# Kernel optimization log

Measured on AMD Instinct MI355X. Metric: run time of the kernel, lower is better.

Reference implementation:

```python
import jax, jax.numpy as jnp
import numpy as np

VOCAB = 150
EOS = 2
PAD = 0
EPS = 1e-8


def _ngram_penalty_sum(tokens, n):
    # tokens: [B, S] int. Returns sum over batch of (count-2)*0.1*n for each
    # ngram repeated >=3 times. Equivalent trick: hash each ngram to a unique
    # int (base-VOCAB encoding), sort per row; a position is a 3rd-or-later
    # occurrence iff sorted[i] == sorted[i-2]; the number of such positions
    # equals sum over unique ngrams of max(count-2, 0).
    B, S = tokens.shape
    if S < n * 3:
        return jnp.float32(0.0)
    L = S - n + 1
    h = sum(tokens[:, j:j + L].astype(jnp.int32) * (VOCAB ** j) for j in range(n))
    hs = jnp.sort(h, axis=1)
    rep = jnp.sum(hs[:, 2:] == hs[:, :-2], axis=1)  # [B]
    return jnp.sum(rep.astype(jnp.float32)) * (0.1 * n)


def setup_inputs() -> dict:
    key = jax.random.key(0)
    k1, k2, k3 = jax.random.split(key, 3)
    B, S, V, IN = 256, 512, VOCAB, 512
    predictions = jax.random.normal(k1, (B, S, V), dtype=jnp.float32)
    targets = jax.random.randint(k2, (B, S), 0, V)
    attention_weights = jax.random.uniform(k3, (B, S, IN), dtype=jnp.float32)
    return {"predictions": predictions, "targets": targets,
            "attention_weights": attention_weights}


def reference(predictions, targets, attention_weights):
    B, S, V = predictions.shape

    # --- main NLL loss (ignore_index=PAD, mean over non-pad) ---
    mask = (targets != PAD).astype(predictions.dtype)  # [B,S]
    gathered = jnp.take_along_axis(predictions, targets[..., None], axis=-1)[..., 0]
    main = -jnp.sum(gathered * mask) / jnp.maximum(jnp.sum(mask), 1.0)

    # --- pattern penalty on argmax tokens ---
    pred_tokens = jnp.argmax(predictions, axis=-1)  # [B,S]
    pattern = (_ngram_penalty_sum(pred_tokens, 2)
               + _ngram_penalty_sum(pred_tokens, 3)
               + _ngram_penalty_sum(pred_tokens, 4)) / B

    # --- EOS encouragement ---
    eos_mask = (targets == EOS).astype(predictions.dtype)  # [B,S]
    eos_probs = jax.nn.softmax(predictions, axis=-1)[:, :, EOS]  # [B,S]
    eos_loss = -jnp.mean(eos_mask * jnp.log(eos_probs + EPS))
    eos_loss = jnp.where(jnp.sum(eos_mask) > 0, eos_loss, 0.0)
    has_eos_t = jnp.any(targets == EOS, axis=1)
    has_eos_p = jnp.any(pred_tokens == EOS, axis=1)
    no_eos = jnp.mean((has_eos_t & ~has_eos_p).astype(predictions.dtype))
    eos_total = eos_loss + 0.5 * no_eos

    # --- attention diversity (negative mean entropy, scaled) ---
    ent = -jnp.sum(attention_weights * jnp.log(attention_weights + EPS), axis=-1)
    attention = -jnp.mean(ent) * 0.1

    total = main + 0.1 * pattern + 0.2 * eos_total + 0.05 * attention
    return jnp.stack([total, main, pattern, eos_total, attention])
```

## Files before the change

### kernel.cpp

```cpp
#include <hip/hip_runtime.h>
#include <math.h>

#define BB   256
#define SS   512
#define VV   150
#define NPOS (BB * SS)
#define GRID 2048
#define EPSF 1e-8f


__device__ __forceinline__ unsigned key32(float f, int idx) {
    const unsigned u = __float_as_uint(f);
    const unsigned mono = ((int)u >= 0) ? (u | 0x80000000u) : ~u;
    return (mono & 0xFFFFFF00u) | (unsigned)(255 - idx);
}

__global__ __launch_bounds__(256) void kern_ab(
    const float* __restrict__ pred, const int* __restrict__ tgt,
    const float* __restrict__ attw, float4* __restrict__ pA,
    float* __restrict__ pB, unsigned char* __restrict__ toks,
    int* __restrict__ counter)
{
    __shared__ float shp[16];
    __shared__ float shb[4];
    const int tid  = threadIdx.x;
    const int lane = tid & 63;
    const int wid  = tid >> 6;

    if (blockIdx.x == 0 && tid == 0) *counter = 0;

    const int gw = blockIdx.x * 4 + wid;
    const float4* a4 = (const float4*)attw;
    const size_t bbase = (size_t)blockIdx.x * 8192;

    float s_g = 0.f, s_mc = 0.f, s_el = 0.f, s_ec = 0.f;
    float s0 = 0.f, s1 = 0.f;

    for (int it = 0; it < 16; ++it) {
        const float4 x0 = a4[bbase + (size_t)(2 * it)     * 256 + tid];
        const float4 x1 = a4[bbase + (size_t)(2 * it + 1) * 256 + tid];

        const int pos = gw + it * 8192;
        const float* row = pred + (size_t)pos * VV;
        const float v0 = row[lane];
        const float v1 = row[lane + 64];
        const bool  l3 = lane < (VV - 128);
        const float v2 = l3 ? row[lane + 128] : -INFINITY;

        unsigned k = key32(v0, lane);
        k = max(k, key32(v1, lane + 64));
        if (l3) k = max(k, key32(v2, lane + 128));
        #pragma unroll
        for (int off = 32; off > 0; off >>= 1)
            k = max(k, __shfl_xor(k, off));
        const int li = 255 - (int)(k & 0xFFu);

        const int t = tgt[pos];
        const float src = (t < 64) ? v0 : (t < 128) ? v1 : v2;
        const float g = __shfl(src, t & 63);

        if (t == 2) {
            const unsigned mono_hi = k & 0xFFFFFF00u;
            const float m = (mono_hi & 0x80000000u)
                          ? __uint_as_float(mono_hi & 0x7FFFFFFFu)
                          : __uint_as_float(~mono_hi);
            float ex = __expf(v0 - m) + __expf(v1 - m)
                     + (l3 ? __expf(v2 - m) : 0.f);
            #pragma unroll
            for (int off = 32; off > 0; off >>= 1)
                ex += __shfl_xor(ex, off);
            const float p2 = __shfl(v0, 2);
            if (lane == 0) {
                s_el += __logf(__expf(p2 - m) / ex + EPSF);
                s_ec += 1.f;
            }
        }
        if (lane == 0) {
            toks[pos] = (unsigned char)li;
            if (t != 0) { s_g += g; s_mc += 1.f; }
        }

        s0 += x0.x * __logf(x0.x + EPSF) + x0.y * __logf(x0.y + EPSF)
            + x0.z * __logf(x0.z + EPSF) + x0.w * __logf(x0.w + EPSF);
        s1 += x1.x * __logf(x1.x + EPSF) + x1.y * __logf(x1.y + EPSF)
            + x1.z * __logf(x1.z + EPSF) + x1.w * __logf(x1.w + EPSF);
    }

    if (lane == 0) {
        shp[wid * 4 + 0] = s_g;  shp[wid * 4 + 1] = s_mc;
        shp[wid * 4 + 2] = s_el; shp[wid * 4 + 3] = s_ec;
    }
    float s = s0 + s1;
    #pragma unroll
    for (int off = 32; off > 0; off >>= 1) s += __shfl_xor(s, off);
    if (lane == 0) shb[wid] = s;

    __syncthreads();
    if (tid == 0) {
        float4 r;
        r.x = shp[0] + shp[4] + shp[8]  + shp[12];
        r.y = shp[1] + shp[5] + shp[9]  + shp[13];
        r.z = shp[2] + shp[6] + shp[10] + shp[14];
        r.w = shp[3] + shp[7] + shp[11] + shp[15];
        pA[blockIdx.x] = r;
        pB[blockIdx.x] = shb[0] + shb[1] + shb[2] + shb[3];
    }
}

__global__ __launch_bounds__(256) void kern_cf(
    const unsigned char* __restrict__ toks, const int* __restrict__ tgt,
    int* __restrict__ pC, int* __restrict__ hasx, int* __restrict__ counter,
    const float4* __restrict__ pA, const float* __restrict__ pB,
    float* __restrict__ out)
{
    const int blk = blockIdx.x;
    const int b = blk & 255;
    const int n = 2 + (blk >> 8);
    const int L = SS - n + 1;
    const int tid = threadIdx.x;

    __shared__ int tok[SS];
    __shared__ __align__(16) int h[SS];
    __shared__ int sflags;
    __shared__ int sticket;

    if (tid == 0) sflags = 0;
    const unsigned char* rt = toks + b * SS;
    tok[tid]       = rt[tid];
    tok[tid + 256] = rt[tid + 256];
    __syncthreads();

    if (blk < 256) {
        const int* trow = tgt + b * SS;
        int f = 0;
        if (trow[tid] == 2 || trow[tid + 256] == 2) f |= 1;
        if (tok[tid] == 2 || tok[tid + 256] == 2)   f |= 2;
        if (f) atomicOr(&sflags, f);
    }

    #pragma unroll
    for (int q = 0; q < 2; ++q) {
        const int i = tid + q * 256;
        int hv;
        if (i < L) {
            hv = tok[i];
            int mul = VV;
            for (int j = 1; j < n; ++j) { hv += tok[i + j] * mul; mul *= VV; }
        } else {
            hv = 0x7F000000 + i;
        }
        h[i] = hv;
    }
    __syncthreads();

    const int i1 = tid, i2 = tid + 256;
    const int h1 = h[i1], h2 = h[i2];
    const int bound1 = (i1 & ~3) + 4;
    const int bound2 = (i2 & ~3) + 4;
    int c1 = 0, c2 = 0;
    for (int j = 0; j < bound1; j += 4) {
        const int4 hv = *(const int4*)&h[j];
        c1 += (hv.x == h1 && j     < i1) + (hv.y == h1 && j + 1 < i1)
            + (hv.z == h1 && j + 2 < i1) + (hv.w == h1 && j + 3 < i1);
    }
    for (int j = 0; j < bound2; j += 4) {
        const int4 hv = *(const int4*)&h[j];
        c2 += (hv.x == h2 && j     < i2) + (hv.y == h2 && j + 1 < i2)
            + (hv.z == h2 && j + 2 < i2) + (hv.w == h2 && j + 3 < i2);
    }
    int rep = (c1 >= 2) + (c2 >= 2);
    #pragma unroll
    for (int off = 32; off > 0; off >>= 1) rep += __shfl_xor(rep, off);
    __shared__ int w4[4];
    if ((tid & 63) == 0) w4[tid >> 6] = rep;
    __syncthreads();
    if (tid == 0) {
        pC[blk] = w4[0] + w4[1] + w4[2] + w4[3];
        if (blk < 256) hasx[b] = ((sflags & 1) && !(sflags & 2)) ? 1 : 0;
        __threadfence();
        sticket = atomicAdd(counter, 1);
    }
    __syncthreads();
    if (sticket != 768 - 1) return;

    __threadfence();
    const int lane = tid & 63;
    const int wid  = tid >> 6;
    double v[9];
    #pragma unroll
    for (int k = 0; k < 9; ++k) v[k] = 0.0;
    for (int i = tid; i < GRID; i += 256) {
        const float4 p = pA[i];
        v[0] += p.x; v[1] += p.y; v[2] += p.z; v[3] += p.w;
    }
    for (int i = tid; i < GRID; i += 256) v[4] += pB[i];
    v[5] = pC[tid]; v[6] = pC[tid + 256]; v[7] = pC[tid + 512];
    v[8] = (double)hasx[tid];

    #pragma unroll
    for (int off = 32; off > 0; off >>= 1)
        #pragma unroll
        for (int k = 0; k < 9; ++k) v[k] += __shfl_xor(v[k], off);

    __shared__ double sd[4][9];
    if (lane == 0)
        for (int k = 0; k < 9; ++k) sd[wid][k] = v[k];
    __syncthreads();

    if (tid == 0) {
        double r[9];
        for (int k = 0; k < 9; ++k) r[k] = sd[0][k] + sd[1][k] + sd[2][k] + sd[3][k];
        const double mainv    = -r[0] / fmax(r[1], 1.0);
        const double eos_loss = (r[3] > 0.0) ? (-r[2] / (double)NPOS) : 0.0;
        const double no_eos   = r[8] / (double)BB;
        const double eos_tot  = eos_loss + 0.5 * no_eos;
        const double att      = 0.1 * r[4] / (double)NPOS;
        const double pattern  = (0.2 * r[5] + 0.3 * r[6] + 0.4 * r[7]) / (double)BB;
        const double total    = mainv + 0.1 * pattern + 0.2 * eos_tot + 0.05 * att;
        out[0] = (float)total;   out[1] = (float)mainv; out[2] = (float)pattern;
        out[3] = (float)eos_tot; out[4] = (float)att;
    }
}

extern "C" void kernel_launch(void* const* d_in, const int* in_sizes, int n_in,
                              void* d_out, int out_size, void* d_ws, size_t ws_size,
                              hipStream_t stream)
{
    const float* pred = (const float*)d_in[0];
    const int*   tgt  = (const int*)d_in[1];
    const float* attw = (const float*)d_in[2];
    float* out = (float*)d_out;
    char*  ws  = (char*)d_ws;

    float4* pA   = (float4*)ws;
    float*  pB   = (float*)(ws + 32768);
    int*    pC   = (int*)(ws + 40960);
    int*    hasx = (int*)(ws + 44032);
    int*    cnt  = (int*)(ws + 45056);
    unsigned char* toks = (unsigned char*)(ws + 45312);

    kern_ab<<<GRID, 256, 0, stream>>>(pred, tgt, attw, pA, pB, toks, cnt);
    kern_cf<<<768, 256, 0, stream>>>(toks, tgt, pC, hasx, cnt, pA, pB, out);
}
```

Measured before the change: 102.1 us.

## Stage prediction rows through LDS with coalesced float4 loads, 16 lanes per row

```diff
diff --git a/kernel.cpp b/kernel.cpp
--- a/kernel.cpp
+++ b/kernel.cpp
@@ -21,6 +21,7 @@
     float* __restrict__ pB, unsigned char* __restrict__ toks,
     int* __restrict__ counter)
 {
+    __shared__ __align__(16) float slab[16 * VV];
     __shared__ float shp[16];
     __shared__ float shb[4];
     const int tid  = threadIdx.x;
@@ -29,71 +30,90 @@
 
     if (blockIdx.x == 0 && tid == 0) *counter = 0;
 
-    const int gw = blockIdx.x * 4 + wid;
-    const float4* a4 = (const float4*)attw;
-    const size_t bbase = (size_t)blockIdx.x * 8192;
-
+    const int s  = tid & 15;
+    const int c0 = s * 10;
+    const int p  = tid >> 4;
     float s_g = 0.f, s_mc = 0.f, s_el = 0.f, s_ec = 0.f;
-    float s0 = 0.f, s1 = 0.f;
-
-    for (int it = 0; it < 16; ++it) {
-        const float4 x0 = a4[bbase + (size_t)(2 * it)     * 256 + tid];
-        const float4 x1 = a4[bbase + (size_t)(2 * it + 1) * 256 + tid];
-
-        const int pos = gw + it * 8192;
-        const float* row = pred + (size_t)pos * VV;
-        const float v0 = row[lane];
-        const float v1 = row[lane + 64];
-        const bool  l3 = lane < (VV - 128);
-        const float v2 = l3 ? row[lane + 128] : -INFINITY;
-
-        unsigned k = key32(v0, lane);
-        k = max(k, key32(v1, lane + 64));
-        if (l3) k = max(k, key32(v2, lane + 128));
-        #pragma unroll
-        for (int off = 32; off > 0; off >>= 1)
-            k = max(k, __shfl_xor(k, off));
-        const int li = 255 - (int)(k & 0xFFu);
-
-        const int t = tgt[pos];
-        const float src = (t < 64) ? v0 : (t < 128) ? v1 : v2;
-        const float g = __shfl(src, t & 63);
-
+
+    for (int it = 0; it < 4; ++it) {
+        const int rbase = blockIdx.x * 64 + it * 16;
+        const float4* g4 = (const float4*)(pred + (size_t)rbase * VV);
+        float4* l4 = (float4*)slab;
+        if (it) __syncthreads();
+        #pragma unroll
+        for (int k = 0; k < 3; ++k) {
+            const int i = tid + k * 256;
+            if (i < 600) l4[i] = g4[i];
+        }
+        __syncthreads();
+
+        const float* row = slab + p * VV;
+        unsigned key = 0;
+        if (s < 15) {
+            const float2* r2 = (const float2*)(row + c0);
+            #pragma unroll
+            for (int j = 0; j < 5; ++j) {
+                const float2 v = r2[j];
+                key = max(key, key32(v.x, c0 + 2 * j));
+                key = max(key, key32(v.y, c0 + 2 * j + 1));
+            }
+        }
+        #pragma unroll
+        for (int off = 1; off <= 8; off <<= 1)
+            key = max(key, __shfl_xor(key, off));
+        const int li = 255 - (int)(key & 0xFFu);
+
+        const int t = tgt[rbase + p];
+        if (t != 0) {
+            if (s == 0)      s_mc += 1.f;
+            if (s == t / 10) s_g += row[t];
+        }
         if (t == 2) {
-            const unsigned mono_hi = k & 0xFFFFFF00u;
+            const unsigned mono_hi = key & 0xFFFFFF00u;
             const float m = (mono_hi & 0x80000000u)
                           ? __uint_as_float(mono_hi & 0x7FFFFFFFu)
                           : __uint_as_float(~mono_hi);
-            float ex = __expf(v0 - m) + __expf(v1 - m)
-                     + (l3 ? __expf(v2 - m) : 0.f);
+            float ex = 0.f;
+            if (s < 15) {
+                #pragma unroll
+                for (int j = 0; j < 10; ++j) ex += __expf(row[c0 + j] - m);
+            }
             #pragma unroll
-            for (int off = 32; off > 0; off >>= 1)
-                ex += __shfl_xor(ex, off);
-            const float p2 = __shfl(v0, 2);
-            if (lane == 0) {
-                s_el += __logf(__expf(p2 - m) / ex + EPSF);
+            for (int off = 1; off <= 8; off <<= 1) ex += __shfl_xor(ex, off);
+            if (s == 0) {
+                s_el += __logf(__expf(row[2] - m) / ex + EPSF);
                 s_ec += 1.f;
             }
         }
-        if (lane == 0) {
-            toks[pos] = (unsigned char)li;
-            if (t != 0) { s_g += g; s_mc += 1.f; }
-        }
-
-        s0 += x0.x * __logf(x0.x + EPSF) + x0.y * __logf(x0.y + EPSF)
-            + x0.z * __logf(x0.z + EPSF) + x0.w * __logf(x0.w + EPSF);
-        s1 += x1.x * __logf(x1.x + EPSF) + x1.y * __logf(x1.y + EPSF)
-            + x1.z * __logf(x1.z + EPSF) + x1.w * __logf(x1.w + EPSF);
-    }
-
+        if (s == 0) toks[rbase + p] = (unsigned char)li;
+    }
+
+    #pragma unroll
+    for (int off = 32; off > 0; off >>= 1) {
+        s_g  += __shfl_xor(s_g,  off);
+        s_mc += __shfl_xor(s_mc, off);
+        s_el += __shfl_xor(s_el, off);
+        s_ec += __shfl_xor(s_ec, off);
+    }
     if (lane == 0) {
         shp[wid * 4 + 0] = s_g;  shp[wid * 4 + 1] = s_mc;
         shp[wid * 4 + 2] = s_el; shp[wid * 4 + 3] = s_ec;
     }
-    float s = s0 + s1;
-    #pragma unroll
-    for (int off = 32; off > 0; off >>= 1) s += __shfl_xor(s, off);
-    if (lane == 0) shb[wid] = s;
+
+    {
+        const float4* a4 = (const float4*)attw;
+        const size_t bbase = (size_t)blockIdx.x * 8192;
+        float sb = 0.f;
+        #pragma unroll 4
+        for (int it = 0; it < 32; ++it) {
+            const float4 v = a4[bbase + it * 256 + tid];
+            sb += v.x * __logf(v.x + EPSF) + v.y * __logf(v.y + EPSF)
+                + v.z * __logf(v.z + EPSF) + v.w * __logf(v.w + EPSF);
+        }
+        #pragma unroll
+        for (int off = 32; off > 0; off >>= 1) sb += __shfl_xor(sb, off);
+        if (lane == 0) shb[wid] = sb;
+    }
 
     __syncthreads();
     if (tid == 0) {
```

Measured after the change: 102.6 us. About the same (+0.5%).
